# Performance work log

Hardware: AMD Instinct MI355X
Metric: run time of the kernel (lower is better)

## Reference

```python
import jax, jax.numpy as jnp
import numpy as np

B, N, EMB, NCLS = 4, 4096, 1024, 13

def knn_euclid(x, k):
    # x: (B,C,N); k nearest by squared euclidean distance
    sq = jnp.sum(x * x, axis=1)                        # (B,N)
    inner = jnp.einsum('bcn,bcm->bnm', x, x)           # (B,N,N)
    d = sq[:, :, None] - 2.0 * inner + sq[:, None, :]
    return jax.lax.stop_gradient(jax.lax.top_k(-d, k)[1])   # (B,N,k)

def knn_cosine(x, k):
    xn = x / (jnp.linalg.norm(x, axis=1, keepdims=True) + 1e-8)
    sim = jnp.einsum('bcn,bcm->bnm', xn, xn)           # (B,N,N)
    return jax.lax.stop_gradient(jax.lax.top_k(sim, k)[1])

def edge_conv(x, idx, w0, s0, o0, w1, s1, o1):
    # x: (B,C,N), idx: (B,N,k) -> (B,64,N). Edge feats = concat(x_j - x_i, x_i).
    xt = jnp.transpose(x, (0, 2, 1))                   # (B,N,C)
    nbr = jax.vmap(lambda f, i: f[i])(xt, idx)         # (B,N,k,C)
    ctr = jnp.broadcast_to(xt[:, :, None, :], nbr.shape)
    e = jnp.concatenate([nbr - ctr, ctr], axis=-1)     # (B,N,k,2C)
    h = jax.nn.leaky_relu(jnp.einsum('bnkc,oc->bnko', e, w0) * s0 + o0, 0.2)
    h = jax.nn.leaky_relu(jnp.einsum('bnkc,oc->bnko', h, w1) * s1 + o1, 0.2)
    return jnp.transpose(jnp.max(h, axis=2), (0, 2, 1))  # max over k -> (B,64,N)

def conv1d(x, w):
    return jnp.einsum('bcn,oc->bon', x, w)

def setup_inputs():
    key = jax.random.key(0)
    cnt = [0]
    def nxt():
        cnt[0] += 1
        return jax.random.fold_in(key, cnt[0])
    W = lambda shape: jax.random.normal(nxt(), shape, jnp.float32) * 0.05
    S = lambda n: 1.0 + 0.1 * jax.random.normal(nxt(), (n,), jnp.float32)   # folded BN scale
    O = lambda n: 0.05 * jax.random.normal(nxt(), (n,), jnp.float32)        # folded BN offset / bias
    inp = {'x': jax.random.normal(nxt(), (B, 6, N), jnp.float32)}
    inp.update(w1_0=W((64, 12)), s1_0=S(64), o1_0=O(64), w1_1=W((64, 64)), s1_1=S(64), o1_1=O(64))
    inp.update(w2_0=W((64, 128)), s2_0=S(64), o2_0=O(64), w2_1=W((64, 64)), s2_1=S(64), o2_1=O(64))
    inp.update(w3_0=W((64, 128)), s3_0=S(64), o3_0=O(64), w3_1=W((64, 64)), s3_1=S(64), o3_1=O(64))
    inp.update(w4=W((EMB, 192)), b4=O(EMB))
    inp.update(wf1=W((512, EMB + 192)), sf1=S(512), of1=O(512))
    inp.update(wf2=W((256, 512)), sf2=S(256), of2=O(256))
    inp.update(wf3=W((NCLS, 256)))
    inp['k'] = 20
    return inp

def reference(x, w1_0, s1_0, o1_0, w1_1, s1_1, o1_1,
              w2_0, s2_0, o2_0, w2_1, s2_1, o2_1,
              w3_0, s3_0, o3_0, w3_1, s3_1, o3_1,
              w4, b4, wf1, sf1, of1, wf2, sf2, of2, wf3, k):
    x1 = edge_conv(x, knn_euclid(x, k), w1_0, s1_0, o1_0, w1_1, s1_1, o1_1)
    x2 = edge_conv(x1, knn_cosine(x1, k), w2_0, s2_0, o2_0, w2_1, s2_1, o2_1)
    x3 = edge_conv(x2, knn_cosine(x2, k), w3_0, s3_0, o3_0, w3_1, s3_1, o3_1)
    xc = jnp.concatenate([x1, x2, x3], axis=1)         # (B,192,N)
    x4 = jax.nn.leaky_relu(conv1d(xc, w4) + b4[None, :, None], 0.2)  # (B,EMB,N)
    g = jnp.max(x4, axis=2, keepdims=True)             # global max pool (B,EMB,1)
    g = jnp.broadcast_to(g, (x4.shape[0], x4.shape[1], xc.shape[2]))  # Repeat to N
    x5 = jnp.concatenate([x1, x2, x3, g], axis=1)      # (B,192+EMB,N)
    h = jax.nn.leaky_relu(conv1d(x5, wf1) * sf1[None, :, None] + of1[None, :, None], 0.2)
    h = jax.nn.leaky_relu(conv1d(h, wf2) * sf2[None, :, None] + of2[None, :, None], 0.2)
    return conv1d(h, wf3)                              # (B,NCLS,N)
```

## Files before the change

kernel.cpp:

```cpp
#include <hip/hip_runtime.h>
#include <hip/hip_bf16.h>
#include <float.h>

#define NPTS 4096
#define NB 4
#define KNN 20

__device__ __forceinline__ float lrelu(float x) { return x > 0.f ? x : 0.2f * x; }

__device__ __forceinline__ void atomicMaxF(float* addr, float val) {
    int* ia = (int*)addr;
    int old = *ia;
    while (__int_as_float(old) < val) {
        int assumed = old;
        old = atomicCAS(ia, assumed, __float_as_int(val));
        if (old == assumed) break;
    }
}

__global__ void k_transp(const float* __restrict__ src, float* __restrict__ dst,
                         int rows, int srcld, int cols) {
    int i = blockIdx.x * 256 + threadIdx.x;
    if (i >= rows * cols) return;
    int r = i % rows, c = i / rows;
    dst[c * rows + r] = src[(size_t)r * srcld + c];
}

__global__ void k_sqnorm(const float* __restrict__ x, float* __restrict__ sq) {
    int i = blockIdx.x * 256 + threadIdx.x;
    int b = i >> 12, n = i & 4095;
    const float* xb = x + b * 6 * NPTS;
    float s = 0.f;
#pragma unroll
    for (int c = 0; c < 6; c++) { float v = xb[c * NPTS + n]; s += v * v; }
    sq[i] = s;
}

__global__ __launch_bounds__(256) void k_knn_euclid(const float* __restrict__ x,
                                                    const float* __restrict__ sq,
                                                    int* __restrict__ idx) {
    int t = threadIdx.x;
    int w = t >> 6, ln = t & 63;
    int qid = blockIdx.x * 4 + w;
    int b = qid >> 12, qn = qid & 4095;
    const float* xb = x + b * 6 * NPTS;
    const float* sqb = sq + b * NPTS;
    float q0 = xb[qn], q1 = xb[NPTS + qn], q2 = xb[2 * NPTS + qn];
    float q3 = xb[3 * NPTS + qn], q4 = xb[4 * NPTS + qn], q5 = xb[5 * NPTS + qn];
    float sqn = sqb[qn];
    float lv = -FLT_MAX; int li = 0x7fffffff;
    float th = -FLT_MAX;
    for (int t0 = 0; t0 < NPTS; t0 += 64) {
        int m = t0 + ln;
        float dot = q0 * xb[m] + q1 * xb[NPTS + m] + q2 * xb[2 * NPTS + m]
                  + q3 * xb[3 * NPTS + m] + q4 * xb[4 * NPTS + m] + q5 * xb[5 * NPTS + m];
        float sv = -(sqn - 2.f * dot + sqb[m]);
        unsigned long long mask = __ballot(sv > th);
        while (mask) {
            int src = __ffsll((unsigned long long)mask) - 1;
            mask &= mask - 1;
            float v = __shfl(sv, src);
            if (!(v > th)) continue;
            int mi = t0 + src;
            float pv = __shfl_up(lv, 1);
            int   pi = __shfl_up(li, 1);
            unsigned long long bm = __ballot(ln < 20 && lv >= v);
            int pos = __popcll(bm);
            if (ln < 20) {
                if (ln == pos) { lv = v; li = mi; }
                else if (ln > pos) { lv = pv; li = pi; }
            }
            th = __shfl(lv, 19);
        }
    }
    if (ln < KNN) idx[qid * KNN + ln] = li;
}

__global__ __launch_bounds__(256) void k_knn_cos(const float* __restrict__ xn,
                                                 const float* __restrict__ xnT,
                                                 int* __restrict__ idx) {
    __shared__ float xq[64][20];
    __shared__ float simb[16][260];
    int t = threadIdx.x;
    int w = t >> 6, ln = t & 63;
    int b = blockIdx.x >> 8;
    int q0blk = (blockIdx.x & 255) * 16;
    const float* xqg = xn + ((size_t)(b << 12) + q0blk) * 64;
    {
        int q = t >> 4, c4 = t & 15;
        float4 v = *(const float4*)(xqg + q * 64 + c4 * 4);
        xq[c4 * 4 + 0][q] = v.x; xq[c4 * 4 + 1][q] = v.y;
        xq[c4 * 4 + 2][q] = v.z; xq[c4 * 4 + 3][q] = v.w;
    }
    __syncthreads();
    int myq = w * 4;
    const float* xTb = xnT + (((size_t)b) << 12) * 64;
    float lv[4] = {-FLT_MAX, -FLT_MAX, -FLT_MAX, -FLT_MAX};
    int   li[4] = {0x7fffffff, 0x7fffffff, 0x7fffffff, 0x7fffffff};
    float th[4] = {-FLT_MAX, -FLT_MAX, -FLT_MAX, -FLT_MAX};
    for (int strip = 0; strip < 16; strip++) {
        int m0 = strip * 256 + ln * 4;
        float4 a[4];
#pragma unroll
        for (int q = 0; q < 4; q++) a[q] = (float4){0, 0, 0, 0};
        for (int c = 0; c < 64; c++) {
            float4 cv = *(const float4*)(xTb + (((size_t)c) << 12) + m0);
            float4 qv = *(const float4*)&xq[c][myq];
            a[0].x += qv.x * cv.x; a[0].y += qv.x * cv.y; a[0].z += qv.x * cv.z; a[0].w += qv.x * cv.w;
            a[1].x += qv.y * cv.x; a[1].y += qv.y * cv.y; a[1].z += qv.y * cv.z; a[1].w += qv.y * cv.w;
            a[2].x += qv.z * cv.x; a[2].y += qv.z * cv.y; a[2].z += qv.z * cv.z; a[2].w += qv.z * cv.w;
            a[3].x += qv.w * cv.x; a[3].y += qv.w * cv.y; a[3].z += qv.w * cv.z; a[3].w += qv.w * cv.w;
        }
#pragma unroll
        for (int q = 0; q < 4; q++)
            *(float4*)&simb[myq + q][ln * 4] = a[q];
#pragma unroll
        for (int q = 0; q < 4; q++) {
            for (int j = 0; j < 4; j++) {
                float sv = simb[myq + q][j * 64 + ln];
                int base = strip * 256 + j * 64;
                unsigned long long mask = __ballot(sv > th[q]);
                while (mask) {
                    int src = __ffsll((unsigned long long)mask) - 1;
                    mask &= mask - 1;
                    float v = __shfl(sv, src);
                    if (!(v > th[q])) continue;
                    int mi = base + src;
                    float pv = __shfl_up(lv[q], 1);
                    int   pi = __shfl_up(li[q], 1);
                    unsigned long long bm = __ballot(ln < 20 && lv[q] >= v);
                    int pos = __popcll(bm);
                    if (ln < 20) {
                        if (ln == pos) { lv[q] = v; li[q] = mi; }
                        else if (ln > pos) { lv[q] = pv; li[q] = pi; }
                    }
                    th[q] = __shfl(lv[q], 19);
                }
            }
        }
    }
#pragma unroll
    for (int q = 0; q < 4; q++) {
        if (ln < KNN) {
            int qid = (b << 12) + q0blk + myq + q;
            idx[(size_t)qid * KNN + ln] = li[q];
        }
    }
}

__global__ void k_normalize(const float* __restrict__ xcpm, int coff,
                            float* __restrict__ xn, float* __restrict__ xnT) {
    int pid = blockIdx.x * 256 + threadIdx.x;
    int b = pid >> 12, n = pid & 4095;
    const float* p = xcpm + (size_t)pid * 192 + coff;
    float s = 0.f;
#pragma unroll
    for (int c4 = 0; c4 < 16; c4++) {
        float4 v = *(const float4*)(p + c4 * 4);
        s += v.x * v.x + v.y * v.y + v.z * v.z + v.w * v.w;
    }
    float inv = 1.f / (sqrtf(s) + 1e-8f);
    float* q = xn + (size_t)pid * 64;
    float* qt = xnT + (((size_t)b) << 12) * 64 + n;
#pragma unroll
    for (int c4 = 0; c4 < 16; c4++) {
        float4 v = *(const float4*)(p + c4 * 4);
        float4 r; r.x = v.x * inv; r.y = v.y * inv; r.z = v.z * inv; r.w = v.w * inv;
        *(float4*)(q + c4 * 4) = r;
        qt[(size_t)(c4 * 4 + 0) << 12] = r.x;
        qt[(size_t)(c4 * 4 + 1) << 12] = r.y;
        qt[(size_t)(c4 * 4 + 2) << 12] = r.z;
        qt[(size_t)(c4 * 4 + 3) << 12] = r.w;
    }
}

__global__ __launch_bounds__(256) void k_edge1(const float* __restrict__ x,
    const float* __restrict__ w0, const float* __restrict__ s0, const float* __restrict__ o0,
    const float* __restrict__ w1, const float* __restrict__ s1, const float* __restrict__ o1,
    const int* __restrict__ idx, float* __restrict__ xcpm) {
    __shared__ float h0s[4][64];
    int t = threadIdx.x;
    int w = t >> 6, o = t & 63;
    int pid = blockIdx.x * 4 + w;
    int pidU = __builtin_amdgcn_readfirstlane(pid);
    int b = pidU >> 12, n = pidU & 4095;
    const float* xb = x + b * 6 * NPTS;
    float w0r[12];
    const float* w0p = w0 + o * 12;
#pragma unroll
    for (int c4 = 0; c4 < 3; c4++) {
        float4 v = *(const float4*)(w0p + c4 * 4);
        w0r[c4 * 4] = v.x; w0r[c4 * 4 + 1] = v.y; w0r[c4 * 4 + 2] = v.z; w0r[c4 * 4 + 3] = v.w;
    }
    float w1r[64];
    const float* w1p = w1 + o * 64;
#pragma unroll
    for (int c4 = 0; c4 < 16; c4++) {
        float4 v = *(const float4*)(w1p + c4 * 4);
        w1r[c4 * 4] = v.x; w1r[c4 * 4 + 1] = v.y; w1r[c4 * 4 + 2] = v.z; w1r[c4 * 4 + 3] = v.w;
    }
    float sv0 = s0[o], ov0 = o0[o], sv1 = s1[o], ov1 = o1[o];
    float h0b = 0.f;
#pragma unroll
    for (int c = 0; c < 6; c++) {
        float cvc = xb[c * NPTS + n];
        h0b += (w0r[6 + c] - w0r[c]) * cvc;
    }
    float acc = -FLT_MAX;
    const int* ib = idx + pidU * KNN;
    for (int kk = 0; kk < KNN; kk++) {
        int j = __builtin_amdgcn_readfirstlane(ib[kk]) & 4095;
        float h = h0b;
#pragma unroll
        for (int c = 0; c < 6; c++) h += w0r[c] * xb[c * NPTS + j];
        h = lrelu(h * sv0 + ov0);
        h0s[w][o] = h;
        float h2 = 0.f;
#pragma unroll
        for (int c4 = 0; c4 < 16; c4++) {
            float4 h4 = *(const float4*)&h0s[w][c4 * 4];
            h2 += w1r[c4 * 4] * h4.x + w1r[c4 * 4 + 1] * h4.y + w1r[c4 * 4 + 2] * h4.z + w1r[c4 * 4 + 3] * h4.w;
        }
        h2 = lrelu(h2 * sv1 + ov1);
        acc = fmaxf(acc, h2);
    }
    xcpm[(size_t)pid * 192 + o] = acc;
}

__global__ __launch_bounds__(256) void k_edge23(const float* __restrict__ xcpm,
    const float* __restrict__ w0, const float* __restrict__ s0, const float* __restrict__ o0,
    const float* __restrict__ w1, const float* __restrict__ s1, const float* __restrict__ o1,
    const int* __restrict__ idx, int ci, int co) {
    __shared__ float h0s[4][64];
    int t = threadIdx.x;
    int w = t >> 6, o = t & 63;
    int pid = blockIdx.x * 4 + w;
    int pidU = __builtin_amdgcn_readfirstlane(pid);
    int b = pidU >> 12;
    float w0r[64];
    const float* w0p = w0 + o * 128;
#pragma unroll
    for (int c4 = 0; c4 < 16; c4++) {
        float4 v = *(const float4*)(w0p + c4 * 4);
        w0r[c4 * 4] = v.x; w0r[c4 * 4 + 1] = v.y; w0r[c4 * 4 + 2] = v.z; w0r[c4 * 4 + 3] = v.w;
    }
    float w1r[64];
    const float* w1p = w1 + o * 64;
#pragma unroll
    for (int c4 = 0; c4 < 16; c4++) {
        float4 v = *(const float4*)(w1p + c4 * 4);
        w1r[c4 * 4] = v.x; w1r[c4 * 4 + 1] = v.y; w1r[c4 * 4 + 2] = v.z; w1r[c4 * 4 + 3] = v.w;
    }
    float sv0 = s0[o], ov0 = o0[o], sv1 = s1[o], ov1 = o1[o];
    const float* cvp = xcpm + (size_t)pidU * 192 + ci;
    const float* w0q = w0p + 64;
    float h0b = 0.f;
#pragma unroll
    for (int c4 = 0; c4 < 16; c4++) {
        float4 wv = *(const float4*)(w0q + c4 * 4);
        float4 cv4 = *(const float4*)(cvp + c4 * 4);
        h0b += (wv.x - w0r[c4 * 4 + 0]) * cv4.x + (wv.y - w0r[c4 * 4 + 1]) * cv4.y
             + (wv.z - w0r[c4 * 4 + 2]) * cv4.z + (wv.w - w0r[c4 * 4 + 3]) * cv4.w;
    }
    float acc = -FLT_MAX;
    const int* ib = idx + pidU * KNN;
    for (int kk = 0; kk < KNN; kk++) {
        int j = __builtin_amdgcn_readfirstlane(ib[kk]) & 4095;
        const float* np = xcpm + ((size_t)(b * 4096 + j)) * 192 + ci;
        float h = h0b;
#pragma unroll
        for (int c4 = 0; c4 < 16; c4++) {
            float4 nv4 = *(const float4*)(np + c4 * 4);
            h += w0r[c4 * 4 + 0] * nv4.x + w0r[c4 * 4 + 1] * nv4.y
               + w0r[c4 * 4 + 2] * nv4.z + w0r[c4 * 4 + 3] * nv4.w;
        }
        h = lrelu(h * sv0 + ov0);
        h0s[w][o] = h;
        float h2 = 0.f;
#pragma unroll
        for (int c4 = 0; c4 < 16; c4++) {
            float4 h4 = *(const float4*)&h0s[w][c4 * 4];
            h2 += w1r[c4 * 4] * h4.x + w1r[c4 * 4 + 1] * h4.y + w1r[c4 * 4 + 2] * h4.z + w1r[c4 * 4 + 3] * h4.w;
        }
        h2 = lrelu(h2 * sv1 + ov1);
        acc = fmaxf(acc, h2);
    }
    float* outp = (float*)xcpm;
    outp[(size_t)pid * 192 + co + o] = acc;
}

__global__ void k_init_g(float* __restrict__ g) {
    g[blockIdx.x * 256 + threadIdx.x] = -FLT_MAX;
}

__global__ __launch_bounds__(256) void k_w4pool(const float* __restrict__ xc,
                                                const float* __restrict__ wT4,
                                                const float* __restrict__ b4,
                                                float* __restrict__ g) {
    __shared__ float xcs[192 * 36];
    int t = threadIdx.x;
    int b = blockIdx.y;
    int n0 = blockIdx.x * 32;
    const float* xb = xc + (size_t)(b * 4096 + n0) * 192;
    for (int i = t; i < 1536; i += 256) {
        int pt = i / 48, c4 = i - pt * 48;
        float4 v = *(const float4*)(xb + pt * 192 + c4 * 4);
        xcs[(c4 * 4 + 0) * 36 + pt] = v.x; xcs[(c4 * 4 + 1) * 36 + pt] = v.y;
        xcs[(c4 * 4 + 2) * 36 + pt] = v.z; xcs[(c4 * 4 + 3) * 36 + pt] = v.w;
    }
    __syncthreads();
    int o0 = (t >> 2) * 16, qd = t & 3;
    float4 bb[4];
#pragma unroll
    for (int k = 0; k < 4; k++) bb[k] = *(const float4*)(b4 + o0 + k * 4);
    float mx[16];
#pragma unroll
    for (int oo = 0; oo < 16; oo++) mx[oo] = -FLT_MAX;
    for (int sub = 0; sub < 2; sub++) {
        int tn0 = sub * 16 + qd * 4;
        float4 acc[16];
#pragma unroll
        for (int oo = 0; oo < 16; oo++) acc[oo] = (float4){0, 0, 0, 0};
        for (int c = 0; c < 192; c++) {
            float4 x4 = *(const float4*)&xcs[c * 36 + tn0];
            const float* wr = wT4 + c * 1024 + o0;
            float4 wq[4];
#pragma unroll
            for (int k = 0; k < 4; k++) wq[k] = *(const float4*)(wr + k * 4);
#pragma unroll
            for (int oo = 0; oo < 16; oo++) {
                float wv = ((const float*)wq)[oo];
                acc[oo].x += wv * x4.x; acc[oo].y += wv * x4.y;
                acc[oo].z += wv * x4.z; acc[oo].w += wv * x4.w;
            }
        }
#pragma unroll
        for (int oo = 0; oo < 16; oo++) {
            float bias = ((const float*)bb)[oo];
            float4 a = acc[oo];
            float h = fmaxf(fmaxf(lrelu(a.x + bias), lrelu(a.y + bias)),
                            fmaxf(lrelu(a.z + bias), lrelu(a.w + bias)));
            mx[oo] = fmaxf(mx[oo], h);
        }
    }
#pragma unroll
    for (int oo = 0; oo < 16; oo++) {
        float v = mx[oo];
        v = fmaxf(v, __shfl_xor(v, 1));
        v = fmaxf(v, __shfl_xor(v, 2));
        if (qd == 0) atomicMaxF(&g[b * 1024 + o0 + oo], v);
    }
}

__global__ __launch_bounds__(256) void k_goff(const float* __restrict__ g,
                                              const float* __restrict__ wf1,
                                              const float* __restrict__ sf1,
                                              const float* __restrict__ of1,
                                              float* __restrict__ goff) {
    int bo = blockIdx.x;
    int b = bo >> 9, o = bo & 511;
    int t = threadIdx.x;
    const float* wr = wf1 + (size_t)o * 1216 + 192;
    const float* gb = g + b * 1024;
    float s = 0.f;
    for (int c = t; c < 1024; c += 256) s += wr[c] * gb[c];
    __shared__ float red[4];
    for (int off = 32; off > 0; off >>= 1) s += __shfl_down(s, off);
    if ((t & 63) == 0) red[t >> 6] = s;
    __syncthreads();
    if (t == 0) {
        float tot = red[0] + red[1] + red[2] + red[3];
        goff[bo] = tot * sf1[o] + of1[o];
    }
}

#define TP 20
__global__ __launch_bounds__(256) void k_tail(const float* __restrict__ xc,
                                              const float* __restrict__ wf1T,
                                              const float* __restrict__ sf1,
                                              const float* __restrict__ goff,
                                              const float* __restrict__ wf2T,
                                              const float* __restrict__ sf2,
                                              const float* __restrict__ of2,
                                              const float* __restrict__ wf3,
                                              float* __restrict__ out) {
    __shared__ float xcs[192 * TP];
    __shared__ float h1s[512 * TP];
    __shared__ float h2s[256 * TP];
    int t = threadIdx.x;
    int b = blockIdx.y;
    int n0 = blockIdx.x * 16;
    const float* xb = xc + (size_t)(b * 4096 + n0) * 192;
    for (int i = t; i < 768; i += 256) {
        int pt = i / 48, c4 = i - pt * 48;
        float4 v = *(const float4*)(xb + pt * 192 + c4 * 4);
        xcs[(c4 * 4 + 0) * TP + pt] = v.x; xcs[(c4 * 4 + 1) * TP + pt] = v.y;
        xcs[(c4 * 4 + 2) * TP + pt] = v.z; xcs[(c4 * 4 + 3) * TP + pt] = v.w;
    }
    __syncthreads();
    {
        int o8 = (t >> 2) * 8, tn0 = (t & 3) * 4;
        float4 acc[8];
#pragma unroll
        for (int oo = 0; oo < 8; oo++) acc[oo] = (float4){0, 0, 0, 0};
        for (int c = 0; c < 192; c++) {
            float4 x4 = *(const float4*)&xcs[c * TP + tn0];
            const float* wr = wf1T + c * 512 + o8;
            float4 w0 = *(const float4*)(wr);
            float4 w1 = *(const float4*)(wr + 4);
            float wq[8] = {w0.x, w0.y, w0.z, w0.w, w1.x, w1.y, w1.z, w1.w};
#pragma unroll
            for (int oo = 0; oo < 8; oo++) {
                acc[oo].x += wq[oo] * x4.x; acc[oo].y += wq[oo] * x4.y;
                acc[oo].z += wq[oo] * x4.z; acc[oo].w += wq[oo] * x4.w;
            }
        }
#pragma unroll
        for (int oo = 0; oo < 8; oo++) {
            int o = o8 + oo;
            float s = sf1[o];
            float gv = goff[b * 512 + o];
            float4 r;
            r.x = lrelu(acc[oo].x * s + gv); r.y = lrelu(acc[oo].y * s + gv);
            r.z = lrelu(acc[oo].z * s + gv); r.w = lrelu(acc[oo].w * s + gv);
            *(float4*)&h1s[o * TP + tn0] = r;
        }
    }
    __syncthreads();
    {
        int o4 = (t >> 2) * 4, tn0 = (t & 3) * 4;
        float4 acc[4];
#pragma unroll
        for (int oo = 0; oo < 4; oo++) acc[oo] = (float4){0, 0, 0, 0};
        for (int c = 0; c < 512; c++) {
            float4 x4 = *(const float4*)&h1s[c * TP + tn0];
            float4 w = *(const float4*)(wf2T + c * 256 + o4);
            float wq[4] = {w.x, w.y, w.z, w.w};
#pragma unroll
            for (int oo = 0; oo < 4; oo++) {
                acc[oo].x += wq[oo] * x4.x; acc[oo].y += wq[oo] * x4.y;
                acc[oo].z += wq[oo] * x4.z; acc[oo].w += wq[oo] * x4.w;
            }
        }
#pragma unroll
        for (int oo = 0; oo < 4; oo++) {
            int o = o4 + oo;
            float s = sf2[o], of = of2[o];
            float4 r;
            r.x = lrelu(acc[oo].x * s + of); r.y = lrelu(acc[oo].y * s + of);
            r.z = lrelu(acc[oo].z * s + of); r.w = lrelu(acc[oo].w * s + of);
            *(float4*)&h2s[o * TP + tn0] = r;
        }
    }
    __syncthreads();
    if (t < 13 * 16) {
        int o = t >> 4, tn = t & 15;
        const float* wr = wf3 + o * 256;
        float acc = 0.f;
        for (int c4 = 0; c4 < 64; c4++) {
            float4 wv = *(const float4*)(wr + c4 * 4);
            acc += wv.x * h2s[(c4 * 4 + 0) * TP + tn] + wv.y * h2s[(c4 * 4 + 1) * TP + tn]
                 + wv.z * h2s[(c4 * 4 + 2) * TP + tn] + wv.w * h2s[(c4 * 4 + 3) * TP + tn];
        }
        out[((size_t)b * 13 + o) * NPTS + n0 + tn] = acc;
    }
}

extern "C" void kernel_launch(void* const* d_in, const int* in_sizes, int n_in,
                              void* d_out, int out_size, void* d_ws, size_t ws_size,
                              hipStream_t stream) {
    const float* x    = (const float*)d_in[0];
    const float* w1_0 = (const float*)d_in[1];
    const float* s1_0 = (const float*)d_in[2];
    const float* o1_0 = (const float*)d_in[3];
    const float* w1_1 = (const float*)d_in[4];
    const float* s1_1 = (const float*)d_in[5];
    const float* o1_1 = (const float*)d_in[6];
    const float* w2_0 = (const float*)d_in[7];
    const float* s2_0 = (const float*)d_in[8];
    const float* o2_0 = (const float*)d_in[9];
    const float* w2_1 = (const float*)d_in[10];
    const float* s2_1 = (const float*)d_in[11];
    const float* o2_1 = (const float*)d_in[12];
    const float* w3_0 = (const float*)d_in[13];
    const float* s3_0 = (const float*)d_in[14];
    const float* o3_0 = (const float*)d_in[15];
    const float* w3_1 = (const float*)d_in[16];
    const float* s3_1 = (const float*)d_in[17];
    const float* o3_1 = (const float*)d_in[18];
    const float* w4   = (const float*)d_in[19];
    const float* b4   = (const float*)d_in[20];
    const float* wf1  = (const float*)d_in[21];
    const float* sf1  = (const float*)d_in[22];
    const float* of1  = (const float*)d_in[23];
    const float* wf2  = (const float*)d_in[24];
    const float* sf2  = (const float*)d_in[25];
    const float* of2  = (const float*)d_in[26];
    const float* wf3  = (const float*)d_in[27];

    float* xcpm = (float*)d_ws;
    float* xn   = xcpm + (size_t)NB * NPTS * 192;
    float* sq   = xn + (size_t)NB * NPTS * 64;
    float* g    = sq + NB * NPTS;
    float* goff = g + NB * 1024;
    int*   idx  = (int*)(goff + NB * 512);
    float* wT4  = (float*)(idx + NB * NPTS * KNN);
    float* wf1T = wT4 + 192 * 1024;
    float* wf2T = wf1T + 192 * 512;
    float* xnT  = wf2T + 512 * 256;
    (void)in_sizes; (void)n_in; (void)out_size; (void)ws_size;

    k_transp<<<(1024 * 192 + 255) / 256, 256, 0, stream>>>(w4, wT4, 1024, 192, 192);
    k_transp<<<(512 * 192 + 255) / 256, 256, 0, stream>>>(wf1, wf1T, 512, 1216, 192);
    k_transp<<<(256 * 512 + 255) / 256, 256, 0, stream>>>(wf2, wf2T, 256, 512, 512);
    k_sqnorm<<<NB * NPTS / 256, 256, 0, stream>>>(x, sq);
    k_knn_euclid<<<NB * NPTS / 4, 256, 0, stream>>>(x, sq, idx);
    k_edge1<<<NB * NPTS / 4, 256, 0, stream>>>(x, w1_0, s1_0, o1_0, w1_1, s1_1, o1_1, idx, xcpm);
    k_normalize<<<NB * NPTS / 256, 256, 0, stream>>>(xcpm, 0, xn, xnT);
    k_knn_cos<<<NB * NPTS / 16, 256, 0, stream>>>(xn, xnT, idx);
    k_edge23<<<NB * NPTS / 4, 256, 0, stream>>>(xcpm, w2_0, s2_0, o2_0, w2_1, s2_1, o2_1, idx, 0, 64);
    k_normalize<<<NB * NPTS / 256, 256, 0, stream>>>(xcpm, 64, xn, xnT);
    k_knn_cos<<<NB * NPTS / 16, 256, 0, stream>>>(xn, xnT, idx);
    k_edge23<<<NB * NPTS / 4, 256, 0, stream>>>(xcpm, w3_0, s3_0, o3_0, w3_1, s3_1, o3_1, idx, 64, 128);
    k_init_g<<<NB * 1024 / 256, 256, 0, stream>>>(g);
    k_w4pool<<<dim3(NPTS / 32, NB), 256, 0, stream>>>(xcpm, wT4, b4, g);
    k_goff<<<NB * 512, 256, 0, stream>>>(g, wf1, sf1, of1, goff);
    k_tail<<<dim3(NPTS / 16, NB), 256, 0, stream>>>(xcpm, wf1T, sf1, goff, wf2T, sf2, of2, wf3, (float*)d_out);
}
```

Measured before the change: 1.587 ms.

## Split cosine kNN candidates into two halves with a merge pass, enlarge w4pool tile

The cosine kNN kernel now has each block scan only half of the candidate points, which doubles the grid to 2048 blocks. Each block writes partial top-20 values and indices to workspace, and a new merge kernel combines the two sorted lists per query. The intent is more parallelism and shorter serial top-k loops per block, at the cost of an extra kernel launch and extra global traffic. Separately, k_w4pool now processes 64 points per block instead of 32, so each weight load is reused across more points and fewer atomic max updates are issued, at the cost of more shared memory and fewer blocks.

New measurement: 1.699 ms. 1.07x slower.

```diff
diff --git a/kernel.cpp b/kernel.cpp
--- a/kernel.cpp
+++ b/kernel.cpp
@@ -78,13 +78,18 @@
 
 __global__ __launch_bounds__(256) void k_knn_cos(const float* __restrict__ xn,
                                                  const float* __restrict__ xnT,
-                                                 int* __restrict__ idx) {
+                                                 float* __restrict__ pval,
+                                                 int* __restrict__ pidx) {
     __shared__ float xq[64][20];
     __shared__ float simb[16][260];
     int t = threadIdx.x;
     int w = t >> 6, ln = t & 63;
-    int b = blockIdx.x >> 8;
-    int q0blk = (blockIdx.x & 255) * 16;
+    int blk = blockIdx.x;
+    int b = blk >> 9;
+    int rem = blk & 511;
+    int half = rem >> 8;
+    int q0blk = (rem & 255) * 16;
+    int cbase = half * 2048;
     const float* xqg = xn + ((size_t)(b << 12) + q0blk) * 64;
     {
         int q = t >> 4, c4 = t & 15;
@@ -98,8 +103,8 @@
     float lv[4] = {-FLT_MAX, -FLT_MAX, -FLT_MAX, -FLT_MAX};
     int   li[4] = {0x7fffffff, 0x7fffffff, 0x7fffffff, 0x7fffffff};
     float th[4] = {-FLT_MAX, -FLT_MAX, -FLT_MAX, -FLT_MAX};
-    for (int strip = 0; strip < 16; strip++) {
-        int m0 = strip * 256 + ln * 4;
+    for (int strip = 0; strip < 8; strip++) {
+        int m0 = cbase + strip * 256 + ln * 4;
         float4 a[4];
 #pragma unroll
         for (int q = 0; q < 4; q++) a[q] = (float4){0, 0, 0, 0};
@@ -118,7 +123,7 @@
         for (int q = 0; q < 4; q++) {
             for (int j = 0; j < 4; j++) {
                 float sv = simb[myq + q][j * 64 + ln];
-                int base = strip * 256 + j * 64;
+                int base = cbase + strip * 256 + j * 64;
                 unsigned long long mask = __ballot(sv > th[q]);
                 while (mask) {
                     int src = __ffsll((unsigned long long)mask) - 1;
@@ -143,8 +148,26 @@
     for (int q = 0; q < 4; q++) {
         if (ln < KNN) {
             int qid = (b << 12) + q0blk + myq + q;
-            idx[(size_t)qid * KNN + ln] = li[q];
-        }
+            pval[(size_t)qid * 40 + half * 20 + ln] = lv[q];
+            pidx[(size_t)qid * 40 + half * 20 + ln] = li[q];
+        }
+    }
+}
+
+__global__ void k_knn_merge(const float* __restrict__ pval, const int* __restrict__ pidx,
+                            int* __restrict__ idx) {
+    int qid = blockIdx.x * 256 + threadIdx.x;
+    const float* va = pval + (size_t)qid * 40;
+    const int* ia_ = pidx + (size_t)qid * 40;
+    int ia = 0, ib = 0;
+    for (int k = 0; k < KNN; k++) {
+        bool takeA;
+        if (ia >= 20) takeA = false;
+        else if (ib >= 20) takeA = true;
+        else takeA = (va[ia] >= va[20 + ib]);
+        int v;
+        if (takeA) { v = ia_[ia]; ia++; } else { v = ia_[20 + ib]; ib++; }
+        idx[(size_t)qid * KNN + k] = v;
     }
 }
 
@@ -297,16 +320,16 @@
                                                 const float* __restrict__ wT4,
                                                 const float* __restrict__ b4,
                                                 float* __restrict__ g) {
-    __shared__ float xcs[192 * 36];
+    __shared__ float xcs[192 * 68];
     int t = threadIdx.x;
     int b = blockIdx.y;
-    int n0 = blockIdx.x * 32;
+    int n0 = blockIdx.x * 64;
     const float* xb = xc + (size_t)(b * 4096 + n0) * 192;
-    for (int i = t; i < 1536; i += 256) {
+    for (int i = t; i < 3072; i += 256) {
         int pt = i / 48, c4 = i - pt * 48;
         float4 v = *(const float4*)(xb + pt * 192 + c4 * 4);
-        xcs[(c4 * 4 + 0) * 36 + pt] = v.x; xcs[(c4 * 4 + 1) * 36 + pt] = v.y;
-        xcs[(c4 * 4 + 2) * 36 + pt] = v.z; xcs[(c4 * 4 + 3) * 36 + pt] = v.w;
+        xcs[(c4 * 4 + 0) * 68 + pt] = v.x; xcs[(c4 * 4 + 1) * 68 + pt] = v.y;
+        xcs[(c4 * 4 + 2) * 68 + pt] = v.z; xcs[(c4 * 4 + 3) * 68 + pt] = v.w;
     }
     __syncthreads();
     int o0 = (t >> 2) * 16, qd = t & 3;
@@ -316,13 +339,13 @@
     float mx[16];
 #pragma unroll
     for (int oo = 0; oo < 16; oo++) mx[oo] = -FLT_MAX;
-    for (int sub = 0; sub < 2; sub++) {
+    for (int sub = 0; sub < 4; sub++) {
         int tn0 = sub * 16 + qd * 4;
         float4 acc[16];
 #pragma unroll
         for (int oo = 0; oo < 16; oo++) acc[oo] = (float4){0, 0, 0, 0};
         for (int c = 0; c < 192; c++) {
-            float4 x4 = *(const float4*)&xcs[c * 36 + tn0];
+            float4 x4 = *(const float4*)&xcs[c * 68 + tn0];
             const float* wr = wT4 + c * 1024 + o0;
             float4 wq[4];
 #pragma unroll
@@ -508,6 +531,8 @@
     float* wf1T = wT4 + 192 * 1024;
     float* wf2T = wf1T + 192 * 512;
     float* xnT  = wf2T + 512 * 256;
+    float* pval = xnT + (size_t)NB * NPTS * 64;
+    int*   pidx = (int*)(pval + (size_t)NB * NPTS * 40);
     (void)in_sizes; (void)n_in; (void)out_size; (void)ws_size;
 
     k_transp<<<(1024 * 192 + 255) / 256, 256, 0, stream>>>(w4, wT4, 1024, 192, 192);
@@ -517,13 +542,15 @@
     k_knn_euclid<<<NB * NPTS / 4, 256, 0, stream>>>(x, sq, idx);
     k_edge1<<<NB * NPTS / 4, 256, 0, stream>>>(x, w1_0, s1_0, o1_0, w1_1, s1_1, o1_1, idx, xcpm);
     k_normalize<<<NB * NPTS / 256, 256, 0, stream>>>(xcpm, 0, xn, xnT);
-    k_knn_cos<<<NB * NPTS / 16, 256, 0, stream>>>(xn, xnT, idx);
+    k_knn_cos<<<NB * 512, 256, 0, stream>>>(xn, xnT, pval, pidx);
+    k_knn_merge<<<NB * NPTS / 256, 256, 0, stream>>>(pval, pidx, idx);
     k_edge23<<<NB * NPTS / 4, 256, 0, stream>>>(xcpm, w2_0, s2_0, o2_0, w2_1, s2_1, o2_1, idx, 0, 64);
     k_normalize<<<NB * NPTS / 256, 256, 0, stream>>>(xcpm, 64, xn, xnT);
-    k_knn_cos<<<NB * NPTS / 16, 256, 0, stream>>>(xn, xnT, idx);
+    k_knn_cos<<<NB * 512, 256, 0, stream>>>(xn, xnT, pval, pidx);
+    k_knn_merge<<<NB * NPTS / 256, 256, 0, stream>>>(pval, pidx, idx);
     k_edge23<<<NB * NPTS / 4, 256, 0, stream>>>(xcpm, w3_0, s3_0, o3_0, w3_1, s3_1, o3_1, idx, 64, 128);
     k_init_g<<<NB * 1024 / 256, 256, 0, stream>>>(g);
-    k_w4pool<<<dim3(NPTS / 32, NB), 256, 0, stream>>>(xcpm, wT4, b4, g);
+    k_w4pool<<<dim3(NPTS / 64, NB), 256, 0, stream>>>(xcpm, wT4, b4, g);
     k_goff<<<NB * 512, 256, 0, stream>>>(g, wf1, sf1, of1, goff);
     k_tail<<<dim3(NPTS / 16, NB), 256, 0, stream>>>(xcpm, wf1T, sf1, goff, wf2T, sf2, of2, wf3, (float*)d_out);
 }
```
